# Kernel tuning notes

Measured on AMD Instinct MI355X. Metric: run time of the kernel, lower is better.

## Reference

```python
import jax, jax.numpy as jnp
import numpy as np
import math

B, S, H = 2, 2048, 2048
NH, HD = 16, 128
THETA = 10000.0
NEG = -1e9


def make_rope_tables(seq_len, head_dim, theta):
    inv_freq = 1.0 / (theta ** (np.arange(0, head_dim, 2, dtype=np.float32) / head_dim))
    pos = np.arange(seq_len, dtype=np.float32)
    freqs = np.outer(pos, inv_freq)                    # (S, HD/2)
    emb = np.concatenate([freqs, freqs], axis=-1)      # (S, HD)
    return jnp.asarray(np.cos(emb)), jnp.asarray(np.sin(emb))


def setup_inputs() -> dict:
    key = jax.random.key(0)
    k1, k2, k3 = jax.random.split(key, 3)
    hidden_states = jax.random.normal(k1, (B, S, H), dtype=jnp.float32)
    rope_cos, rope_sin = make_rope_tables(S, HD, THETA)
    # additive causal mask [1,1,S,S]
    causal = jnp.tril(jnp.ones((S, S), dtype=bool))
    attention_mask = jnp.where(causal, 0.0, NEG).astype(jnp.float32)[None, None]
    w_qkv = jax.random.normal(k2, (3 * H, H), dtype=jnp.float32) * (1.0 / math.sqrt(H))
    w_o = jax.random.normal(k3, (H, H), dtype=jnp.float32) * (1.0 / math.sqrt(H))
    return {"hidden_states": hidden_states, "rope_cos": rope_cos, "rope_sin": rope_sin,
            "attention_mask": attention_mask, "w_qkv": w_qkv, "w_o": w_o}


def apply_rope(x, cos, sin):
    # x: (B, NH, S, HD); cos/sin: (S, HD)
    half = x.shape[-1] // 2
    x1, x2 = x[..., :half], x[..., half:]
    x_rot = jnp.concatenate([-x2, x1], axis=-1)
    return x * cos[None, None] + x_rot * sin[None, None]


def reference(hidden_states, rope_cos, rope_sin, attention_mask, w_qkv, w_o):
    b, s, h = hidden_states.shape
    qkv = hidden_states @ w_qkv.T                      # (B, S, 3H)
    qkv = qkv.reshape(b, s, 3, NH, HD).transpose(2, 0, 3, 1, 4)  # (3, B, NH, S, HD)
    q, k, v = qkv[0], qkv[1], qkv[2]
    q = apply_rope(q, rope_cos, rope_sin)
    k = apply_rope(k, rope_cos, rope_sin)
    scale = 1.0 / math.sqrt(HD)
    scores = jnp.einsum('bhqd,bhkd->bhqk', q, k) * scale + attention_mask
    probs = jax.nn.softmax(scores.astype(jnp.float32), axis=-1).astype(q.dtype)
    out = jnp.einsum('bhqk,bhkd->bhqd', probs, v)      # (B, NH, S, HD)
    out = out.transpose(0, 2, 1, 3).reshape(b, s, h)
    return out @ w_o.T
```

## Files before the change

### kernel.cpp

```cpp
#include <hip/hip_runtime.h>
#include <stdint.h>

typedef unsigned int u32;
typedef unsigned short u16;

typedef __bf16 bf16x8 __attribute__((ext_vector_type(8)));
typedef float f32x4 __attribute__((ext_vector_type(4)));

struct alignas(16) V16 { u32 a, b, c, d; };

__device__ __forceinline__ u16 f2bf(float x) {
    u32 u = __float_as_uint(x);
    u += 0x7FFFu + ((u >> 16) & 1u);
    return (u16)(u >> 16);
}
__device__ __forceinline__ float bf2f(u16 h) {
    return __uint_as_float(((u32)h) << 16);
}

__device__ __forceinline__ bf16x8 ld_frag(const u16* p) {
    return __builtin_bit_cast(bf16x8, *(const V16*)p);
}

__device__ __forceinline__ void async_cp16(u16* lds_dst, const u16* g_src) {
    __builtin_amdgcn_global_load_lds(
        (__attribute__((address_space(1))) void*)g_src,
        (__attribute__((address_space(3))) void*)lds_dst, 16, 0, 0);
}

__global__ __launch_bounds__(256) void cast_all_kernel(
    const float* __restrict__ hidden, const float* __restrict__ wqkv,
    const float* __restrict__ wo,
    u16* __restrict__ hA, u16* __restrict__ wqb, u16* __restrict__ wob)
{
    int i = blockIdx.x * 256 + threadIdx.x;
    const float* src; u16* dst; int off;
    if (i < 2097152)      { src = hidden; dst = hA;  off = i; }
    else if (i < 5242880) { src = wqkv;   dst = wqb; off = i - 2097152; }
    else                  { src = wo;     dst = wob; off = i - 5242880; }
    const float* p = src + (size_t)off * 4;
    ushort4 o;
    o.x = f2bf(p[0]); o.y = f2bf(p[1]); o.z = f2bf(p[2]); o.w = f2bf(p[3]);
    *(ushort4*)(dst + (size_t)off * 4) = o;
}

__device__ __forceinline__ void stage_half(
    u16* smem, const u16* __restrict__ Ag, const u16* __restrict__ Bg,
    int K, int isB, int kk, int buf, int th, int w, int rg0, int chl)
{
    const u16* G = isB ? Bg : Ag;
    u16* base = smem + isB * 32768 + buf * 16384 + kk * 8192;
    const int kcol = th * 64 + kk * 32;
#pragma unroll
    for (int i = 0; i < 2; ++i) {
        const int s = i * 8 + w;
        const int rg = s * 16 + rg0;
        async_cp16(base + s * 512, G + (size_t)rg * K + kcol + chl * 8);
    }
}

__global__ __launch_bounds__(512, 2) void gemm256(
    const u16* __restrict__ A, const u16* __restrict__ Bt,
    int M, int N, int K, int mode,
    float* __restrict__ Cout,
    u16* __restrict__ Qb, u16* __restrict__ Kb, u16* __restrict__ Vtb,
    const float* __restrict__ cosT, const float* __restrict__ sinT, float qscale)
{
    extern __shared__ u16 smem[];
    const int t = threadIdx.x;
    const int w = t >> 6, l = t & 63;
    const int lr = l & 15, lk = (l >> 4) * 8;
    const int wm16 = (w >> 2) * 8;
    const int wn16 = (w & 3) * 4;
    const int laneoff = lr * 32 + (lk ^ ((lr & 8) ? 16 : 0));
    const int rg0 = l >> 2;
    const int chl = (l & 3) ^ ((l >> 4) & 2);

    const int flat = blockIdx.y * gridDim.x + blockIdx.x;
    const int xcd = flat & 7, slot = flat >> 3;
    const int cpx = gridDim.x >> 3;
    const int ncol = xcd * cpx + slot % cpx;
    const int mrow = slot / cpx;
    const int m0 = mrow * 256, n0 = ncol * 256;

    const u16* Ag = A + (size_t)m0 * K;
    const u16* Bg = Bt + (size_t)n0 * K;

    f32x4 acc[8][4];
#pragma unroll
    for (int i = 0; i < 8; ++i)
#pragma unroll
        for (int j = 0; j < 4; ++j) acc[i][j] = f32x4{0.f, 0.f, 0.f, 0.f};

    const int NT = K >> 6;

    stage_half(smem, Ag, Bg, K, 0, 0, 0, 0, w, rg0, chl);
    stage_half(smem, Ag, Bg, K, 1, 0, 0, 0, w, rg0, chl);
    stage_half(smem, Ag, Bg, K, 0, 1, 0, 0, w, rg0, chl);
    stage_half(smem, Ag, Bg, K, 1, 1, 0, 0, w, rg0, chl);
    stage_half(smem, Ag, Bg, K, 0, 0, 1, 1, w, rg0, chl);
    stage_half(smem, Ag, Bg, K, 1, 0, 1, 1, w, rg0, chl);
    asm volatile("s_waitcnt vmcnt(8)" ::: "memory");
    __builtin_amdgcn_s_barrier();

    for (int tt = 0; tt < NT; tt += 2) {
#pragma unroll
        for (int sub = 0; sub < 2; ++sub) {
            const int tcur = tt + sub;
            const u16* Abuf = smem + sub * 16384;
            const u16* Bbuf = smem + 32768 + sub * 16384;
            bf16x8 bfr[4];
#pragma unroll
            for (int p = 0; p < 4; ++p) {
                const int kk = p >> 1, mh = p & 1;
                const u16* Ab = Abuf + kk * 8192;
                const u16* Bb = Bbuf + kk * 8192;
                if (mh == 0) {
#pragma unroll
                    for (int ni = 0; ni < 4; ++ni)
                        bfr[ni] = ld_frag(Bb + (wn16 + ni) * 512 + laneoff);
                }
                bf16x8 af[4];
#pragma unroll
                for (int i = 0; i < 4; ++i)
                    af[i] = ld_frag(Ab + (wm16 + mh * 4 + i) * 512 + laneoff);

                if (p == 0 && tcur + 1 < NT)
                    stage_half(smem, Ag, Bg, K, 0, 1, sub ^ 1, tcur + 1, w, rg0, chl);
                if (p == 1 && tcur + 1 < NT)
                    stage_half(smem, Ag, Bg, K, 1, 1, sub ^ 1, tcur + 1, w, rg0, chl);
                if (p == 2 && tcur + 2 < NT)
                    stage_half(smem, Ag, Bg, K, 0, 0, sub, tcur + 2, w, rg0, chl);
                if (p == 3 && tcur + 2 < NT)
                    stage_half(smem, Ag, Bg, K, 1, 0, sub, tcur + 2, w, rg0, chl);

                if (p == 1) {
                    if (tcur < NT - 1) asm volatile("s_waitcnt vmcnt(8)" ::: "memory");
                    else               asm volatile("s_waitcnt vmcnt(0)" ::: "memory");
                }
                if (p == 3) {
                    if (tcur < NT - 2)       asm volatile("s_waitcnt vmcnt(8)" ::: "memory");
                    else if (tcur == NT - 2) asm volatile("s_waitcnt vmcnt(4)" ::: "memory");
                }
                __builtin_amdgcn_s_barrier();
                __builtin_amdgcn_s_setprio(1);
#pragma unroll
                for (int i = 0; i < 4; ++i)
#pragma unroll
                    for (int ni = 0; ni < 4; ++ni)
                        acc[mh * 4 + i][ni] = __builtin_amdgcn_mfma_f32_16x16x32_bf16(
                            af[i], bfr[ni], acc[mh * 4 + i][ni], 0, 0, 0);
                __builtin_amdgcn_s_setprio(0);
                __builtin_amdgcn_s_barrier();
            }
        }
    }

    __syncthreads();
    const int lrow4 = (l >> 4) * 4;
    const int wm0 = (w >> 2) * 128, wn0 = (w & 3) * 64;

    if (mode == 1) {
#pragma unroll
        for (int mi = 0; mi < 8; ++mi)
#pragma unroll
            for (int ni = 0; ni < 4; ++ni)
#pragma unroll
                for (int r = 0; r < 4; ++r) {
                    int gr = m0 + wm0 + mi * 16 + lrow4 + r;
                    int gc = n0 + wn0 + ni * 16 + lr;
                    Cout[(size_t)gr * N + gc] = acc[mi][ni][r];
                }
        return;
    }

    const int which = n0 >> 11;
    const int nh0 = (n0 & 2047) >> 7;
    const int bb = m0 >> 11;
    const int s0 = m0 & 2047;

    if (which < 2) {
#pragma unroll
        for (int mi = 0; mi < 8; ++mi)
#pragma unroll
            for (int ni = 0; ni < 4; ++ni)
#pragma unroll
                for (int r = 0; r < 4; ++r)
                    smem[(wm0 + mi * 16 + lrow4 + r) * 256 + wn0 + ni * 16 + lr] =
                        f2bf(acc[mi][ni][r]);
    } else {
#pragma unroll
        for (int mi = 0; mi < 8; ++mi)
#pragma unroll
            for (int ni = 0; ni < 4; ++ni)
#pragma unroll
                for (int r = 0; r < 4; ++r) {
                    int cr = wn0 + ni * 16 + lr;
                    int cc = wm0 + mi * 16 + lrow4 + r;
                    smem[cr * 256 + (cc ^ ((cr & 7) << 3))] = f2bf(acc[mi][ni][r]);
                }
    }
    __syncthreads();

    if (which < 2) {
        const bool isQ = (which == 0);
        u16* dstb = isQ ? Qb : Kb;
        const float qs = isQ ? qscale : 1.0f;
#pragma unroll
        for (int ps = 0; ps < 16; ++ps) {
            int chunk = ps * 512 + t;
            int row = chunk >> 5;
            int ce = (chunk & 31) * 8;
            int head = nh0 + (ce >> 7);
            int d = ce & 127;
            union { V16 v; u16 h[8]; } xv, pv, ov;
            xv.v = *(const V16*)&smem[row * 256 + ce];
            pv.v = *(const V16*)&smem[row * 256 + (ce ^ 64)];
            const float* cp = cosT + (size_t)(s0 + row) * 128 + d;
            const float* sp = sinT + (size_t)(s0 + row) * 128 + d;
            const float sgn = (d < 64) ? -1.f : 1.f;
#pragma unroll
            for (int i = 0; i < 8; ++i) {
                float x  = bf2f(xv.h[i]);
                float xr = bf2f(pv.h[i]);
                ov.h[i] = f2bf((x * cp[i] + sgn * xr * sp[i]) * qs);
            }
            *(V16*)&dstb[((size_t)(bb * 16 + head) * 2048 + s0 + row) * 128 + d] = ov.v;
        }
    } else {
#pragma unroll
        for (int ps = 0; ps < 16; ++ps) {
            int chunk = ps * 512 + t;
            int drow = chunk >> 5;
            int se = (chunk & 31) * 8;
            int head = nh0 + (drow >> 7);
            int d = drow & 127;
            *(V16*)&Vtb[((size_t)(bb * 16 + head) * 128 + d) * 2048 + s0 + se] =
                *(const V16*)&smem[drow * 256 + (se ^ ((drow & 7) << 3))];
        }
    }
}

__global__ __launch_bounds__(256) void gemm_bt(
    const u16* __restrict__ A, const u16* __restrict__ Bt,
    int M, int N, int K,
    float* __restrict__ Cout)
{
    __shared__ u16 smem[16384];
    u16* As = smem;
    u16* Bs = smem + 8192;

    const int t = threadIdx.x;
    const int w = t >> 6, l = t & 63;
    const int lr = l & 15;
    const int lk = (l >> 4) * 8;

    const int flat = blockIdx.y * gridDim.x + blockIdx.x;
    const int xcd = flat & 7, slot = flat >> 3;
    const int cpx = gridDim.x >> 3;
    const int ncol = xcd * cpx + slot % cpx;
    const int mrow = slot / cpx;
    const int m0 = mrow * 128, n0 = ncol * 128;
    const int wm = (w >> 1) * 64, wn = (w & 1) * 64;

    f32x4 acc[4][4];
#pragma unroll
    for (int i = 0; i < 4; ++i)
#pragma unroll
        for (int j = 0; j < 4; ++j) acc[i][j] = f32x4{0.f, 0.f, 0.f, 0.f};

    const u16* Ag = A + (size_t)m0 * K;
    const u16* Bg = Bt + (size_t)n0 * K;
    const int srow = l >> 2;
    const int scol = (l & 3) * 8;

    for (int k0 = 0; k0 < K; k0 += 64) {
#pragma unroll
        for (int g = 0; g < 2; ++g) {
            const int row = w * 32 + g * 16;
#pragma unroll
            for (int c = 0; c < 2; ++c) {
                async_cp16(&As[c * 4096 + row * 32],
                           Ag + (size_t)(row + srow) * K + k0 + c * 32 + scol);
                async_cp16(&Bs[c * 4096 + row * 32],
                           Bg + (size_t)(row + srow) * K + k0 + c * 32 + scol);
            }
        }
        __syncthreads();

#pragma unroll
        for (int c = 0; c < 2; ++c) {
            bf16x8 af[4], bf[4];
#pragma unroll
            for (int i = 0; i < 4; ++i)
                af[i] = ld_frag(&As[c * 4096 + (wm + i * 16 + lr) * 32 + lk]);
#pragma unroll
            for (int j = 0; j < 4; ++j)
                bf[j] = ld_frag(&Bs[c * 4096 + (wn + j * 16 + lr) * 32 + lk]);
#pragma unroll
            for (int i = 0; i < 4; ++i)
#pragma unroll
                for (int j = 0; j < 4; ++j)
                    acc[i][j] = __builtin_amdgcn_mfma_f32_16x16x32_bf16(af[i], bf[j], acc[i][j], 0, 0, 0);
        }
        __syncthreads();
    }

    const int lrow4 = (l >> 4) * 4;
#pragma unroll
    for (int i = 0; i < 4; ++i)
#pragma unroll
        for (int j = 0; j < 4; ++j)
#pragma unroll
            for (int r = 0; r < 4; ++r) {
                int gr = m0 + wm + i * 16 + lrow4 + r;
                int gc = n0 + wn + j * 16 + lr;
                Cout[(size_t)gr * N + gc] = acc[i][j][r];
            }
}

#define PS_LD 72
__global__ __launch_bounds__(256, 2) void flash_attn(
    const u16* __restrict__ Qb, const u16* __restrict__ Kb, const u16* __restrict__ Vtb,
    u16* __restrict__ ctx)
{
    __shared__ u16 Ks[64 * 128];
    __shared__ u16 Vts[128 * 64];
    __shared__ u16 Ps[4 * 16 * PS_LD];

    const int t = threadIdx.x, w = t >> 6, l = t & 63;
    const int lr = l & 15, lk = (l >> 4) * 8, lrow4 = (l >> 4) * 4;
    const int hi = l >> 4;
    const int xw = lr & 7;
    const int bh = blockIdx.x;
    const int pidx = blockIdx.y;
    const int wm = w * 16;

    const u16* Qg = Qb + (size_t)bh * 2048 * 128;
    const u16* Kg = Kb + (size_t)bh * 2048 * 128;
    const u16* Vg = Vtb + (size_t)bh * 128 * 2048;
    u16* Pw = &Ps[w * 16 * PS_LD];

    const int krow_l = l >> 4;
    const int vrow_l = l >> 3;
    const int vchk = ((l & 7) ^ vrow_l) * 8;

    const int b = bh >> 4, nh = bh & 15;

#pragma unroll
    for (int half = 0; half < 2; ++half) {
        const int qt = half ? pidx : 31 - pidx;
        const int q0 = qt * 64;

        bf16x8 qfrag[4];
#pragma unroll
        for (int kc = 0; kc < 4; ++kc)
            qfrag[kc] = ld_frag(&Qg[(size_t)(q0 + wm + lr) * 128 + kc * 32 + lk]);

        f32x4 oacc[8];
#pragma unroll
        for (int jo = 0; jo < 8; ++jo) oacc[jo] = f32x4{0.f, 0.f, 0.f, 0.f};
        float l_part[4] = {0.f, 0.f, 0.f, 0.f};

        const int ktiles = qt + 1;
        for (int kt = 0; kt < ktiles; ++kt) {
            const int c0 = kt * 64;
#pragma unroll
            for (int it = 0; it < 4; ++it) {
                const int krow = it * 4 + krow_l;
                const int kchk = ((l & 15) ^ (krow & 7)) * 8;
                async_cp16(&Ks[w * 2048 + it * 512],
                           Kg + (size_t)(c0 + w * 16 + krow) * 128 + kchk);
            }
#pragma unroll
            for (int it = 0; it < 4; ++it) {
                const int vrow = w * 32 + it * 8 + vrow_l;
                async_cp16(&Vts[w * 2048 + it * 512],
                           Vg + (size_t)vrow * 2048 + c0 + vchk);
            }
            __syncthreads();

            f32x4 pacc[4];
#pragma unroll
            for (int j = 0; j < 4; ++j) pacc[j] = f32x4{0.f, 0.f, 0.f, 0.f};
#pragma unroll
            for (int kc = 0; kc < 4; ++kc) {
                const int kco = ((kc * 4 + hi) ^ xw) * 8;
                bf16x8 bk[4];
#pragma unroll
                for (int j = 0; j < 4; ++j)
                    bk[j] = ld_frag(&Ks[(j * 16 + lr) * 128 + kco]);
#pragma unroll
                for (int j = 0; j < 4; ++j)
                    pacc[j] = __builtin_amdgcn_mfma_f32_16x16x32_bf16(qfrag[kc], bk[j], pacc[j], 0, 0, 0);
            }

            if (kt == qt) {
#pragma unroll
                for (int j = 0; j < 4; ++j) {
                    const int cl = j * 16 + lr;
#pragma unroll
                    for (int r = 0; r < 4; ++r) {
                        float pv = (cl > wm + lrow4 + r) ? 0.f : __expf(pacc[j][r]);
                        pacc[j][r] = pv;
                        l_part[r] += pv;
                    }
                }
            } else {
#pragma unroll
                for (int j = 0; j < 4; ++j)
#pragma unroll
                    for (int r = 0; r < 4; ++r) {
                        float pv = __expf(pacc[j][r]);
                        pacc[j][r] = pv;
                        l_part[r] += pv;
                    }
            }

#pragma unroll
            for (int j = 0; j < 4; ++j)
#pragma unroll
                for (int r = 0; r < 4; ++r)
                    Pw[(lrow4 + r) * PS_LD + j * 16 + lr] = f2bf(pacc[j][r]);

#pragma unroll
            for (int kc = 0; kc < 2; ++kc) {
                bf16x8 ap = ld_frag(&Pw[lr * PS_LD + kc * 32 + lk]);
                const int vco = ((kc * 4 + hi) ^ xw) * 8;
#pragma unroll
                for (int jo = 0; jo < 8; ++jo) {
                    bf16x8 bv = ld_frag(&Vts[(jo * 16 + lr) * 64 + vco]);
                    oacc[jo] = __builtin_amdgcn_mfma_f32_16x16x32_bf16(ap, bv, oacc[jo], 0, 0, 0);
                }
            }
            __syncthreads();
        }

        float linv[4];
#pragma unroll
        for (int r = 0; r < 4; ++r) {
            float s = l_part[r];
#pragma unroll
            for (int dd = 8; dd >= 1; dd >>= 1) s += __shfl_xor(s, dd);
            linv[r] = __builtin_amdgcn_rcpf(s);
        }
#pragma unroll
        for (int jo = 0; jo < 8; ++jo)
#pragma unroll
            for (int r = 0; r < 4; ++r) {
                int srow2 = q0 + wm + lrow4 + r;
                int col = nh * 128 + jo * 16 + lr;
                ctx[((size_t)b * 2048 + srow2) * 2048 + col] = f2bf(oacc[jo][r] * linv[r]);
            }
    }
}

extern "C" void kernel_launch(void* const* d_in, const int* in_sizes, int n_in,
                              void* d_out, int out_size, void* d_ws, size_t ws_size,
                              hipStream_t stream)
{
    (void)in_sizes; (void)n_in; (void)out_size; (void)ws_size;
    const float* hidden = (const float*)d_in[0];
    const float* cosT   = (const float*)d_in[1];
    const float* sinT   = (const float*)d_in[2];
    const float* wqkv   = (const float*)d_in[4];
    const float* wo     = (const float*)d_in[5];
    float* out = (float*)d_out;
    char* ws = (char*)d_ws;

    u16* hA   = (u16*)(ws + 0);
    u16* wqb  = (u16*)(ws + 16777216);
    u16* wob  = (u16*)(ws + 41943040);
    u16* Qb   = (u16*)(ws + 50331648);
    u16* Kb   = (u16*)(ws + 67108864);
    u16* Vtb  = (u16*)(ws + 83886080);
    u16* ctx  = (u16*)(ws + 100663296);

    static bool attr_done = false;
    if (!attr_done) {
        hipFuncSetAttribute((const void*)gemm256,
                            hipFuncAttributeMaxDynamicSharedMemorySize, 131072);
        attr_done = true;
    }

    cast_all_kernel<<<dim3(24576), dim3(256), 0, stream>>>(hidden, wqkv, wo,
                                                           hA, wqb, wob);

    gemm256<<<dim3(24, 16), dim3(512), 131072, stream>>>(
        hA, wqb, 4096, 6144, 2048, 0, nullptr, Qb, Kb, Vtb,
        cosT, sinT, 0.08838834764831845f);

    flash_attn<<<dim3(32, 16), dim3(256), 0, stream>>>(Qb, Kb, Vtb, ctx);

    gemm_bt<<<dim3(16, 32), dim3(256), 0, stream>>>(ctx, wob, 4096, 2048, 2048, out);
}
```

Baseline: 379.3 us.

## Replace output-projection GEMM with double-buffered 256x128 pipelined MFMA kernel

```diff
diff --git a/kernel.cpp b/kernel.cpp
--- a/kernel.cpp
+++ b/kernel.cpp
@@ -61,8 +61,7 @@
 
 __global__ __launch_bounds__(512, 2) void gemm256(
     const u16* __restrict__ A, const u16* __restrict__ Bt,
-    int M, int N, int K, int mode,
-    float* __restrict__ Cout,
+    int M, int N, int K,
     u16* __restrict__ Qb, u16* __restrict__ Kb, u16* __restrict__ Vtb,
     const float* __restrict__ cosT, const float* __restrict__ sinT, float qscale)
 {
@@ -159,20 +158,6 @@
     __syncthreads();
     const int lrow4 = (l >> 4) * 4;
     const int wm0 = (w >> 2) * 128, wn0 = (w & 3) * 64;
-
-    if (mode == 1) {
-#pragma unroll
-        for (int mi = 0; mi < 8; ++mi)
-#pragma unroll
-            for (int ni = 0; ni < 4; ++ni)
-#pragma unroll
-                for (int r = 0; r < 4; ++r) {
-                    int gr = m0 + wm0 + mi * 16 + lrow4 + r;
-                    int gc = n0 + wn0 + ni * 16 + lr;
-                    Cout[(size_t)gr * N + gc] = acc[mi][ni][r];
-                }
-        return;
-    }
 
     const int which = n0 >> 11;
     const int nh0 = (n0 & 2047) >> 7;
@@ -241,80 +226,145 @@
     }
 }
 
-__global__ __launch_bounds__(256) void gemm_bt(
+__device__ __forceinline__ void stage_A(
+    u16* smem, const u16* __restrict__ Ag, int K,
+    int kk, int buf, int tile, int w, int rg0, int chl)
+{
+    u16* base = smem + buf * 16384 + kk * 8192;
+    const int kcol = tile * 64 + kk * 32 + chl * 8;
+#pragma unroll
+    for (int i = 0; i < 2; ++i) {
+        const int s = i * 8 + w;
+        async_cp16(base + s * 512, Ag + (size_t)(s * 16 + rg0) * K + kcol);
+    }
+}
+__device__ __forceinline__ void stage_B(
+    u16* smem, const u16* __restrict__ Bg, int K,
+    int kk, int buf, int tile, int w, int rg0, int chl)
+{
+    u16* base = smem + 32768 + buf * 8192 + kk * 4096;
+    const int kcol = tile * 64 + kk * 32 + chl * 8;
+    async_cp16(base + w * 512, Bg + (size_t)(w * 16 + rg0) * K + kcol);
+}
+
+__global__ __launch_bounds__(512, 2) void gemm_mn(
     const u16* __restrict__ A, const u16* __restrict__ Bt,
     int M, int N, int K,
     float* __restrict__ Cout)
 {
-    __shared__ u16 smem[16384];
-    u16* As = smem;
-    u16* Bs = smem + 8192;
-
+    extern __shared__ u16 smem[];
     const int t = threadIdx.x;
     const int w = t >> 6, l = t & 63;
-    const int lr = l & 15;
-    const int lk = (l >> 4) * 8;
+    const int lr = l & 15, lk = (l >> 4) * 8;
+    const int wmr = w >> 1, wnc = w & 1;
+    const int wmr4 = wmr * 4, wnc4 = wnc * 4;
+    const int laneoff = lr * 32 + (lk ^ ((lr & 8) ? 16 : 0));
+    const int rg0 = l >> 2;
+    const int chl = (l & 3) ^ ((l >> 4) & 2);
 
     const int flat = blockIdx.y * gridDim.x + blockIdx.x;
     const int xcd = flat & 7, slot = flat >> 3;
     const int cpx = gridDim.x >> 3;
     const int ncol = xcd * cpx + slot % cpx;
     const int mrow = slot / cpx;
-    const int m0 = mrow * 128, n0 = ncol * 128;
-    const int wm = (w >> 1) * 64, wn = (w & 1) * 64;
-
-    f32x4 acc[4][4];
-#pragma unroll
-    for (int i = 0; i < 4; ++i)
-#pragma unroll
-        for (int j = 0; j < 4; ++j) acc[i][j] = f32x4{0.f, 0.f, 0.f, 0.f};
+    const int m0 = mrow * 256, n0 = ncol * 128;
 
     const u16* Ag = A + (size_t)m0 * K;
     const u16* Bg = Bt + (size_t)n0 * K;
-    const int srow = l >> 2;
-    const int scol = (l & 3) * 8;
-
-    for (int k0 = 0; k0 < K; k0 += 64) {
-#pragma unroll
-        for (int g = 0; g < 2; ++g) {
-            const int row = w * 32 + g * 16;
-#pragma unroll
-            for (int c = 0; c < 2; ++c) {
-                async_cp16(&As[c * 4096 + row * 32],
-                           Ag + (size_t)(row + srow) * K + k0 + c * 32 + scol);
-                async_cp16(&Bs[c * 4096 + row * 32],
-                           Bg + (size_t)(row + srow) * K + k0 + c * 32 + scol);
-            }
-        }
-        __syncthreads();
-
-#pragma unroll
-        for (int c = 0; c < 2; ++c) {
-            bf16x8 af[4], bf[4];
+
+    f32x4 acc[4][4];
+#pragma unroll
+    for (int i = 0; i < 4; ++i)
+#pragma unroll
+        for (int j = 0; j < 4; ++j) acc[i][j] = f32x4{0.f, 0.f, 0.f, 0.f};
+
+    const int NT = K >> 6;
+
+    stage_A(smem, Ag, K, 0, 0, 0, w, rg0, chl);
+    stage_B(smem, Bg, K, 0, 0, 0, w, rg0, chl);
+    stage_A(smem, Ag, K, 1, 0, 0, w, rg0, chl);
+    stage_B(smem, Bg, K, 1, 0, 0, w, rg0, chl);
+    stage_A(smem, Ag, K, 0, 1, 1, w, rg0, chl);
+    stage_B(smem, Bg, K, 0, 1, 1, w, rg0, chl);
+    asm volatile("s_waitcnt vmcnt(6)" ::: "memory");
+    __builtin_amdgcn_s_barrier();
+
+    bf16x8 af0[4], bf0[4], af1[4], bf1[4];
+#pragma unroll
+    for (int i = 0; i < 4; ++i)
+        af0[i] = ld_frag(smem + (wmr4 + i) * 512 + laneoff);
+#pragma unroll
+    for (int j = 0; j < 4; ++j)
+        bf0[j] = ld_frag(smem + 32768 + (wnc4 + j) * 512 + laneoff);
+
+    for (int tt = 0; tt < NT; ++tt) {
+        const int bsel = tt & 1;
+        const u16* Ab  = smem + bsel * 16384;
+        const u16* Bb  = smem + 32768 + bsel * 8192;
+        const u16* AbN = smem + (bsel ^ 1) * 16384;
+        const u16* BbN = smem + 32768 + (bsel ^ 1) * 8192;
+
+        if (tt + 1 < NT) {
+            stage_A(smem, Ag, K, 1, bsel ^ 1, tt + 1, w, rg0, chl);
+            stage_B(smem, Bg, K, 1, bsel ^ 1, tt + 1, w, rg0, chl);
+        }
+        if (tt < NT - 1) asm volatile("s_waitcnt vmcnt(6)" ::: "memory");
+        else             asm volatile("s_waitcnt vmcnt(0)" ::: "memory");
+        __builtin_amdgcn_s_barrier();
+        __builtin_amdgcn_s_setprio(1);
+#pragma unroll
+        for (int i = 0; i < 4; ++i)
+            af1[i] = ld_frag(Ab + 8192 + (wmr4 + i) * 512 + laneoff);
+#pragma unroll
+        for (int j = 0; j < 4; ++j)
+            bf1[j] = ld_frag(Bb + 4096 + (wnc4 + j) * 512 + laneoff);
+        __builtin_amdgcn_sched_barrier(0);
+#pragma unroll
+        for (int i = 0; i < 4; ++i)
+#pragma unroll
+            for (int j = 0; j < 4; ++j)
+                acc[i][j] = __builtin_amdgcn_mfma_f32_16x16x32_bf16(
+                    af0[i], bf0[j], acc[i][j], 0, 0, 0);
+        __builtin_amdgcn_s_setprio(0);
+        __builtin_amdgcn_s_barrier();
+
+        if (tt + 2 < NT) {
+            stage_A(smem, Ag, K, 0, bsel, tt + 2, w, rg0, chl);
+            stage_B(smem, Bg, K, 0, bsel, tt + 2, w, rg0, chl);
+        }
+        if (tt < NT - 2)       asm volatile("s_waitcnt vmcnt(6)" ::: "memory");
+        else if (tt == NT - 2) asm volatile("s_waitcnt vmcnt(3)" ::: "memory");
+        __builtin_amdgcn_s_barrier();
+        __builtin_amdgcn_s_setprio(1);
+        if (tt + 1 < NT) {
 #pragma unroll
             for (int i = 0; i < 4; ++i)
-                af[i] = ld_frag(&As[c * 4096 + (wm + i * 16 + lr) * 32 + lk]);
+                af0[i] = ld_frag(AbN + (wmr4 + i) * 512 + laneoff);
 #pragma unroll
             for (int j = 0; j < 4; ++j)
-                bf[j] = ld_frag(&Bs[c * 4096 + (wn + j * 16 + lr) * 32 + lk]);
-#pragma unroll
-            for (int i = 0; i < 4; ++i)
-#pragma unroll
-                for (int j = 0; j < 4; ++j)
-                    acc[i][j] = __builtin_amdgcn_mfma_f32_16x16x32_bf16(af[i], bf[j], acc[i][j], 0, 0, 0);
-        }
-        __syncthreads();
+                bf0[j] = ld_frag(BbN + (wnc4 + j) * 512 + laneoff);
+        }
+        __builtin_amdgcn_sched_barrier(0);
+#pragma unroll
+        for (int i = 0; i < 4; ++i)
+#pragma unroll
+            for (int j = 0; j < 4; ++j)
+                acc[i][j] = __builtin_amdgcn_mfma_f32_16x16x32_bf16(
+                    af1[i], bf1[j], acc[i][j], 0, 0, 0);
+        __builtin_amdgcn_s_setprio(0);
+        __builtin_amdgcn_s_barrier();
     }
 
     const int lrow4 = (l >> 4) * 4;
+    const int rb = wmr * 64, cb = wnc * 64;
 #pragma unroll
     for (int i = 0; i < 4; ++i)
 #pragma unroll
         for (int j = 0; j < 4; ++j)
 #pragma unroll
             for (int r = 0; r < 4; ++r) {
-                int gr = m0 + wm + i * 16 + lrow4 + r;
-                int gc = n0 + wn + j * 16 + lr;
+                int gr = m0 + rb + i * 16 + lrow4 + r;
+                int gc = n0 + cb + j * 16 + lr;
                 Cout[(size_t)gr * N + gc] = acc[i][j][r];
             }
 }
@@ -480,6 +530,8 @@
     if (!attr_done) {
         hipFuncSetAttribute((const void*)gemm256,
                             hipFuncAttributeMaxDynamicSharedMemorySize, 131072);
+        hipFuncSetAttribute((const void*)gemm_mn,
+                            hipFuncAttributeMaxDynamicSharedMemorySize, 98304);
         attr_done = true;
     }
 
@@ -487,10 +539,11 @@
                                                            hA, wqb, wob);
 
     gemm256<<<dim3(24, 16), dim3(512), 131072, stream>>>(
-        hA, wqb, 4096, 6144, 2048, 0, nullptr, Qb, Kb, Vtb,
+        hA, wqb, 4096, 6144, 2048, Qb, Kb, Vtb,
         cosT, sinT, 0.08838834764831845f);
 
     flash_attn<<<dim3(32, 16), dim3(256), 0, stream>>>(Qb, Kb, Vtb, ctx);
 
-    gemm_bt<<<dim3(16, 32), dim3(256), 0, stream>>>(ctx, wob, 4096, 2048, 2048, out);
-}
+    gemm_mn<<<dim3(16, 16), dim3(512), 98304, stream>>>(
+        ctx, wob, 4096, 2048, 2048, out);
+}
```

Measured after the change: 378.9 us. Within noise of the previous version (-0.1%).
